# Kernel tuning notes

Measured on AMD Instinct MI355X. Metric: run time of the kernel, lower is better.

Reference implementation:

```python
import jax, jax.numpy as jnp
import numpy as np
import math

D_MODEL = 1024
N_HEADS = 16
HEAD_DIM = D_MODEL // N_HEADS
BATCH = 2
SEQ = 2048


def setup_inputs() -> dict:
    key = jax.random.key(0)
    ks = jax.random.split(key, 6)
    x = jax.random.normal(ks[0], (BATCH, SEQ, D_MODEL), dtype=jnp.float32)
    # causal additive mask, finite large negative
    causal = jnp.tril(jnp.ones((SEQ, SEQ), dtype=bool))
    attn_mask = jnp.where(causal, 0.0, -1e9).astype(jnp.float32)[None, None, :, :]
    s = 1.0 / math.sqrt(D_MODEL)
    W_qkv = jax.random.uniform(ks[1], (3 * D_MODEL, D_MODEL), jnp.float32, -s, s)
    b_qkv = jax.random.uniform(ks[2], (3 * D_MODEL,), jnp.float32, -s, s)
    W_out = jax.random.uniform(ks[3], (D_MODEL, D_MODEL), jnp.float32, -s, s)
    b_out = jax.random.uniform(ks[4], (D_MODEL,), jnp.float32, -s, s)
    return {"x": x, "attn_mask": attn_mask, "W_qkv": W_qkv, "b_qkv": b_qkv,
            "W_out": W_out, "b_out": b_out}


def reference(x, attn_mask, W_qkv, b_qkv, W_out, b_out):
    batch, seq, _ = x.shape
    # torch Linear: x @ W^T + b
    qkv = x @ W_qkv.T + b_qkv                              # [B,S,3D]
    qkv = qkv.reshape(batch, seq, 3, N_HEADS, HEAD_DIM)
    qkv = jnp.transpose(qkv, (2, 0, 3, 1, 4))              # [3,B,H,S,hd]
    q, k, v = qkv[0], qkv[1], qkv[2]
    scores = jnp.einsum('bhsd,bhtd->bhst', q, k) / math.sqrt(HEAD_DIM)
    scores = scores + attn_mask
    attn = jax.nn.softmax(scores, axis=-1)                 # dropout p=0 (eval)
    context = jnp.einsum('bhst,bhtd->bhsd', attn, v)       # [B,H,S,hd]
    context = jnp.transpose(context, (0, 2, 1, 3)).reshape(batch, seq, D_MODEL)
    return context @ W_out.T + b_out
```

## Files before the change

### kernel.cpp

```cpp
#include <hip/hip_runtime.h>
#include <hip/hip_bf16.h>

#define BATCH 2
#define SEQ 2048
#define DMODEL 1024
#define NHEADS 16
#define HDIM 64
#define MROWS (BATCH*SEQ)

typedef short bf16x8_t __attribute__((ext_vector_type(8)));
typedef float f32x4_t __attribute__((ext_vector_type(4)));

union Frag { uint4 u; bf16x8_t b; };

__device__ __forceinline__ unsigned short f2bf(float f) {
  union { __hip_bfloat16 h; unsigned short s; } u;
  u.h = __float2bfloat16(f);
  return u.s;
}

__device__ __forceinline__ void gload16(const unsigned short* g, unsigned short* l) {
  __builtin_amdgcn_global_load_lds(
      (const __attribute__((address_space(1))) unsigned int*)(const void*)g,
      (__attribute__((address_space(3))) unsigned int*)(void*)l,
      16, 0, 0);
}

__global__ void cvt_kernel(const float* __restrict__ in,
                           unsigned short* __restrict__ out, int n4) {
  for (int i = blockIdx.x * blockDim.x + threadIdx.x; i < n4;
       i += gridDim.x * blockDim.x) {
    float4 v = reinterpret_cast<const float4*>(in)[i];
    ushort4 o;
    o.x = f2bf(v.x); o.y = f2bf(v.y); o.z = f2bf(v.z); o.w = f2bf(v.w);
    reinterpret_cast<ushort4*>(out)[i] = o;
  }
}

#define QSCALE 0.18033688011112042f


__launch_bounds__(256)
__global__ void qkv_gemm_kernel(const unsigned short* __restrict__ A,
                                const unsigned short* __restrict__ Bw,
                                const float* __restrict__ bias,
                                unsigned short* __restrict__ qb,
                                unsigned short* __restrict__ kb,
                                unsigned short* __restrict__ vb) {
  __shared__ __align__(16) unsigned short As[128 * 32];
  __shared__ __align__(16) unsigned short Bs[128 * 32];
  const int tid = threadIdx.x;
  const int w = tid >> 6, lane = tid & 63;
  const int rr = lane & 15, cg = lane >> 4;
  const int wr = w >> 1, wc = w & 1;
  const int bm = blockIdx.x * 128, bn = blockIdx.y * 128;

  const int cid0 = (w * 2) * 64 + lane, cid1 = (w * 2 + 1) * 64 + lane;
  const int rowA0 = cid0 >> 2, kc0 = cid0 & 3;
  const int rowA1 = cid1 >> 2, kc1 = cid1 & 3;
  const unsigned short* gA0 = A + (size_t)(bm + rowA0) * DMODEL + kc0 * 8;
  const unsigned short* gA1 = A + (size_t)(bm + rowA1) * DMODEL + kc1 * 8;
  const unsigned short* gB0 = Bw + (size_t)(bn + rowA0) * DMODEL + kc0 * 8;
  const unsigned short* gB1 = Bw + (size_t)(bn + rowA1) * DMODEL + kc1 * 8;
  unsigned short* lA0 = As + (w * 2) * 512;
  unsigned short* lA1 = As + (w * 2 + 1) * 512;
  unsigned short* lB0 = Bs + (w * 2) * 512;
  unsigned short* lB1 = Bs + (w * 2 + 1) * 512;

  f32x4_t acc[4][4];
#pragma unroll
  for (int i = 0; i < 4; ++i)
#pragma unroll
    for (int j = 0; j < 4; ++j) acc[i][j] = (f32x4_t){0.f, 0.f, 0.f, 0.f};

  for (int k0 = 0; k0 < DMODEL; k0 += 32) {
    __syncthreads();
    gload16(gA0 + k0, lA0);
    gload16(gA1 + k0, lA1);
    gload16(gB0 + k0, lB0);
    gload16(gB1 + k0, lB1);
    __syncthreads();
    const uint4* A4 = reinterpret_cast<const uint4*>(As);
    const uint4* B4 = reinterpret_cast<const uint4*>(Bs);
    Frag af[4], bf[4];
#pragma unroll
    for (int mt = 0; mt < 4; ++mt) af[mt].u = A4[(wr * 64 + 16 * mt + rr) * 4 + cg];
#pragma unroll
    for (int nt = 0; nt < 4; ++nt) bf[nt].u = B4[(wc * 64 + 16 * nt + rr) * 4 + cg];
#pragma unroll
    for (int mt = 0; mt < 4; ++mt)
#pragma unroll
      for (int nt = 0; nt < 4; ++nt)
        acc[mt][nt] = __builtin_amdgcn_mfma_f32_16x16x32_bf16(af[mt].b, bf[nt].b, acc[mt][nt], 0, 0, 0);
  }

#pragma unroll
  for (int nt = 0; nt < 4; ++nt) {
    const int m = bn + wc * 64 + 16 * nt + rr;
    const float bv = bias[m];
    const int which = m >> 10;
    const int h = (m & 1023) >> 6;
    const int d = m & 63;
#pragma unroll
    for (int mt = 0; mt < 4; ++mt) {
#pragma unroll
      for (int r = 0; r < 4; ++r) {
        const int n = bm + wr * 64 + 16 * mt + cg * 4 + r;
        const int b = n >> 11, sq = n & (SEQ - 1);
        const int bh = b * NHEADS + h;
        float val = acc[mt][nt][r] + bv;
        if (which == 0) {
          qb[((size_t)bh * SEQ + sq) * HDIM + d] = f2bf(val * QSCALE);
        } else if (which == 1) {
          kb[((size_t)bh * SEQ + sq) * HDIM + d] = f2bf(val);
        } else {
          vb[((size_t)bh * HDIM + d) * SEQ + sq] = f2bf(val);
        }
      }
    }
  }
}

__launch_bounds__(256)
__global__ void out_gemm_kernel(const unsigned short* __restrict__ A,
                                const unsigned short* __restrict__ Bw,
                                const float* __restrict__ bias,
                                float* __restrict__ out) {
  __shared__ __align__(16) unsigned short As[128 * 32];
  __shared__ __align__(16) unsigned short Bs[128 * 32];
  const int tid = threadIdx.x;
  const int w = tid >> 6, lane = tid & 63;
  const int rr = lane & 15, cg = lane >> 4;
  const int wr = w >> 1, wc = w & 1;
  const int bm = blockIdx.x * 128, bn = blockIdx.y * 128;

  const int cid0 = (w * 2) * 64 + lane, cid1 = (w * 2 + 1) * 64 + lane;
  const int rowA0 = cid0 >> 2, kc0 = cid0 & 3;
  const int rowA1 = cid1 >> 2, kc1 = cid1 & 3;
  const unsigned short* gA0 = A + (size_t)(bm + rowA0) * DMODEL + kc0 * 8;
  const unsigned short* gA1 = A + (size_t)(bm + rowA1) * DMODEL + kc1 * 8;
  const unsigned short* gB0 = Bw + (size_t)(bn + rowA0) * DMODEL + kc0 * 8;
  const unsigned short* gB1 = Bw + (size_t)(bn + rowA1) * DMODEL + kc1 * 8;
  unsigned short* lA0 = As + (w * 2) * 512;
  unsigned short* lA1 = As + (w * 2 + 1) * 512;
  unsigned short* lB0 = Bs + (w * 2) * 512;
  unsigned short* lB1 = Bs + (w * 2 + 1) * 512;

  f32x4_t acc[4][4];
#pragma unroll
  for (int i = 0; i < 4; ++i)
#pragma unroll
    for (int j = 0; j < 4; ++j) acc[i][j] = (f32x4_t){0.f, 0.f, 0.f, 0.f};

  for (int k0 = 0; k0 < DMODEL; k0 += 32) {
    __syncthreads();
    gload16(gA0 + k0, lA0);
    gload16(gA1 + k0, lA1);
    gload16(gB0 + k0, lB0);
    gload16(gB1 + k0, lB1);
    __syncthreads();
    const uint4* A4 = reinterpret_cast<const uint4*>(As);
    const uint4* B4 = reinterpret_cast<const uint4*>(Bs);
    Frag af[4], bf[4];
#pragma unroll
    for (int mt = 0; mt < 4; ++mt) af[mt].u = A4[(wr * 64 + 16 * mt + rr) * 4 + cg];
#pragma unroll
    for (int nt = 0; nt < 4; ++nt) bf[nt].u = B4[(wc * 64 + 16 * nt + rr) * 4 + cg];
#pragma unroll
    for (int mt = 0; mt < 4; ++mt)
#pragma unroll
      for (int nt = 0; nt < 4; ++nt)
        acc[mt][nt] = __builtin_amdgcn_mfma_f32_16x16x32_bf16(af[mt].b, bf[nt].b, acc[mt][nt], 0, 0, 0);
  }

#pragma unroll
  for (int nt = 0; nt < 4; ++nt) {
    const int m = bn + wc * 64 + 16 * nt + rr;
    const float bv = bias[m];
#pragma unroll
    for (int mt = 0; mt < 4; ++mt) {
#pragma unroll
      for (int r = 0; r < 4; ++r) {
        const int n = bm + wr * 64 + 16 * mt + cg * 4 + r;
        out[(size_t)n * DMODEL + m] = acc[mt][nt][r] + bv;
      }
    }
  }
}

__launch_bounds__(256)
__global__ void attn_kernel(const unsigned short* __restrict__ qb,
                            const unsigned short* __restrict__ kb,
                            const unsigned short* __restrict__ vb,
                            unsigned short* __restrict__ ctx) {
  __shared__ __align__(16) uint4 Ks[2][512];
  __shared__ __align__(16) uint4 Vs[2][512];
  __shared__ __align__(16) uint4 Ps[4][128];

  const int tid = threadIdx.x;
  const int w = tid >> 6, lane = tid & 63;
  const int rr = lane & 15, cg = lane >> 4;
  const int rxw = rr & 7;
  const int p = blockIdx.x;
  const int bh = blockIdx.y;

  const unsigned short* Kbh = kb + (size_t)bh * SEQ * HDIM;
  const unsigned short* Vbh = vb + (size_t)bh * HDIM * SEQ;

  const int j0 = w * 2, j1 = w * 2 + 1;
  const int cid0 = j0 * 64 + lane, cid1 = j1 * 64 + lane;
  const int row0 = cid0 >> 3, ch0 = cid0 & 7;
  const int row1 = cid1 >> 3, ch1 = cid1 & 7;
  const int kOff0 = row0 * HDIM + ((ch0 ^ (row0 & 7)) << 3);
  const int kOff1 = row1 * HDIM + ((ch1 ^ (row1 & 7)) << 3);
  const int vOff0 = row0 * SEQ + ((ch0 ^ (row0 & 7)) << 3);
  const int vOff1 = row1 * SEQ + ((ch1 ^ (row1 & 7)) << 3);

  unsigned short* Pw16 = (unsigned short*)&Ps[w][0];
  const uint4* PwU4 = &Ps[w][0];

#define STAGE(bi, tb_) do {                                             \
    const unsigned short* Kt_ = Kbh + (size_t)(tb_) * HDIM;             \
    const unsigned short* Vt_ = Vbh + (tb_);                            \
    unsigned short* kl_ = (unsigned short*)&Ks[bi][0];                  \
    unsigned short* vl_ = (unsigned short*)&Vs[bi][0];                  \
    gload16(Kt_ + kOff0, kl_ + j0 * 512);                               \
    gload16(Kt_ + kOff1, kl_ + j1 * 512);                               \
    gload16(Vt_ + vOff0, vl_ + j0 * 512);                               \
    gload16(Vt_ + vOff1, vl_ + j1 * 512);                               \
  } while (0)

  const int b = bh >> 4, h = bh & 15;

  for (int ci = 0; ci < 2; ++ci) {
    const int c = (ci == 0) ? p : 31 - p;
    const int s_base = c * 64 + w * 16;
    const int nt = c + 1;

    __syncthreads();
    STAGE(0, 0);

    Frag q0, q1;
    {
      const unsigned short* qrow = qb + ((size_t)bh * SEQ + (s_base + rr)) * HDIM;
      q0.u = *reinterpret_cast<const uint4*>(qrow + cg * 8);
      q1.u = *reinterpret_cast<const uint4*>(qrow + 32 + cg * 8);
    }

    f32x4_t acc[4];
#pragma unroll
    for (int i = 0; i < 4; ++i) acc[i] = (f32x4_t){0.f, 0.f, 0.f, 0.f};
    float mreg[4] = {-1e30f, -1e30f, -1e30f, -1e30f};
    float lp[4] = {0.f, 0.f, 0.f, 0.f};

    for (int t = 0; t < nt; ++t) {
      const int tb = t * 64;
      __syncthreads();
      if (t + 1 < nt) STAGE((t + 1) & 1, (t + 1) * 64);
      if (tb > s_base + 15) continue;
      const bool last = (t == nt - 1);
      const uint4* Kt = &Ks[t & 1][0];
      const uint4* Vt = &Vs[t & 1][0];

      f32x4_t s[4];
      __builtin_amdgcn_s_setprio(1);
#pragma unroll
      for (int st = 0; st < 4; ++st) {
        s[st] = (f32x4_t){0.f, 0.f, 0.f, 0.f};
        Frag kf;
        kf.u = Kt[(st * 16 + rr) * 8 + (cg ^ rxw)];
        s[st] = __builtin_amdgcn_mfma_f32_16x16x32_bf16(q0.b, kf.b, s[st], 0, 0, 0);
        kf.u = Kt[(st * 16 + rr) * 8 + ((4 + cg) ^ rxw)];
        s[st] = __builtin_amdgcn_mfma_f32_16x16x32_bf16(q1.b, kf.b, s[st], 0, 0, 0);
      }
      __builtin_amdgcn_s_setprio(0);

      if (last) {
#pragma unroll
        for (int st = 0; st < 4; ++st) {
          const int keyl = st * 16 + rr;
#pragma unroll
          for (int r = 0; r < 4; ++r)
            if (keyl > w * 16 + cg * 4 + r) s[st][r] = -1e30f;
        }
      }

      float mx[4];
      int need = 0;
#pragma unroll
      for (int r = 0; r < 4; ++r) {
        mx[r] = fmaxf(fmaxf(s[0][r], s[1][r]), fmaxf(s[2][r], s[3][r]));
        need |= (mx[r] > mreg[r] + 11.0f);
      }
      if (__any(need)) {
#pragma unroll
        for (int r = 0; r < 4; ++r) {
          float m = mx[r];
#pragma unroll
          for (int o = 1; o < 16; o <<= 1) m = fmaxf(m, __shfl_xor(m, o));
          m = fmaxf(m, mreg[r]);
          const float alpha = exp2f(mreg[r] - m);
          mreg[r] = m;
          lp[r] *= alpha;
#pragma unroll
          for (int dt = 0; dt < 4; ++dt) acc[dt][r] *= alpha;
        }
      }
#pragma unroll
      for (int r = 0; r < 4; ++r) {
        const float p0 = exp2f(s[0][r] - mreg[r]);
        const float p1 = exp2f(s[1][r] - mreg[r]);
        const float p2 = exp2f(s[2][r] - mreg[r]);
        const float p3 = exp2f(s[3][r] - mreg[r]);
        lp[r] += (p0 + p1) + (p2 + p3);
        const int prow = cg * 4 + r;
        unsigned short* Pr = Pw16 + prow * 64;
        const int swz = (prow & 7) << 3;
        Pr[(rr)      ^ swz] = f2bf(p0);
        Pr[(rr + 16) ^ swz] = f2bf(p1);
        Pr[(rr + 32) ^ swz] = f2bf(p2);
        Pr[(rr + 48) ^ swz] = f2bf(p3);
      }

      Frag pf0, pf1;
      pf0.u = PwU4[rr * 8 + (cg ^ rxw)];
      pf1.u = PwU4[rr * 8 + ((4 + cg) ^ rxw)];
      __builtin_amdgcn_s_setprio(1);
#pragma unroll
      for (int dt = 0; dt < 4; ++dt) {
        Frag vf;
        vf.u = Vt[(dt * 16 + rr) * 8 + (cg ^ rxw)];
        acc[dt] = __builtin_amdgcn_mfma_f32_16x16x32_bf16(pf0.b, vf.b, acc[dt], 0, 0, 0);
        vf.u = Vt[(dt * 16 + rr) * 8 + ((4 + cg) ^ rxw)];
        acc[dt] = __builtin_amdgcn_mfma_f32_16x16x32_bf16(pf1.b, vf.b, acc[dt], 0, 0, 0);
      }
      __builtin_amdgcn_s_setprio(0);
    }

#pragma unroll
    for (int r = 0; r < 4; ++r) {
      float ls = lp[r];
#pragma unroll
      for (int o = 1; o < 16; o <<= 1) ls += __shfl_xor(ls, o);
      const float inv = 1.0f / ls;
      const int sq = s_base + cg * 4 + r;
      unsigned short* crow = ctx + (size_t)(b * SEQ + sq) * DMODEL + h * HDIM;
#pragma unroll
      for (int dt = 0; dt < 4; ++dt)
        crow[dt * 16 + rr] = f2bf(acc[dt][r] * inv);
    }
  }
#undef STAGE
}

extern "C" void kernel_launch(void* const* d_in, const int* in_sizes, int n_in,
                              void* d_out, int out_size, void* d_ws, size_t ws_size,
                              hipStream_t stream) {
  const float* x    = (const float*)d_in[0];
  const float* Wqkv = (const float*)d_in[2];
  const float* bqkv = (const float*)d_in[3];
  const float* Wout = (const float*)d_in[4];
  const float* bout = (const float*)d_in[5];
  float* out = (float*)d_out;

  unsigned short* ws    = (unsigned short*)d_ws;
  unsigned short* xb    = ws;
  unsigned short* wqkvb = xb + (size_t)MROWS * DMODEL;
  unsigned short* woutb = wqkvb + (size_t)3 * DMODEL * DMODEL;
  unsigned short* qbuf  = woutb + (size_t)DMODEL * DMODEL;
  unsigned short* kbuf  = qbuf + (size_t)BATCH * NHEADS * SEQ * HDIM;
  unsigned short* vbuf  = kbuf + (size_t)BATCH * NHEADS * SEQ * HDIM;
  unsigned short* ctx   = vbuf + (size_t)BATCH * NHEADS * SEQ * HDIM;

  cvt_kernel<<<1024, 256, 0, stream>>>(x, xb, MROWS * DMODEL / 4);
  cvt_kernel<<<1024, 256, 0, stream>>>(Wqkv, wqkvb, 3 * DMODEL * DMODEL / 4);
  cvt_kernel<<<256, 256, 0, stream>>>(Wout, woutb, DMODEL * DMODEL / 4);

  qkv_gemm_kernel<<<dim3(MROWS / 128, 3 * DMODEL / 128), 256, 0, stream>>>(
      xb, wqkvb, bqkv, qbuf, kbuf, vbuf);

  attn_kernel<<<dim3(SEQ / 128, BATCH * NHEADS), 256, 0, stream>>>(
      qbuf, kbuf, vbuf, ctx);

  out_gemm_kernel<<<dim3(MROWS / 128, DMODEL / 128), 256, 0, stream>>>(
      ctx, woutb, bout, out);
}
```

Measured before the change: 131.4 us.

## Compute transposed S in attention, pass P via permlane swaps, one chunk per block

```diff
diff --git a/kernel.cpp b/kernel.cpp
--- a/kernel.cpp
+++ b/kernel.cpp
@@ -188,21 +188,20 @@
   }
 }
 
-__launch_bounds__(256)
+__launch_bounds__(256, 4)
 __global__ void attn_kernel(const unsigned short* __restrict__ qb,
                             const unsigned short* __restrict__ kb,
                             const unsigned short* __restrict__ vb,
                             unsigned short* __restrict__ ctx) {
   __shared__ __align__(16) uint4 Ks[2][512];
   __shared__ __align__(16) uint4 Vs[2][512];
-  __shared__ __align__(16) uint4 Ps[4][128];
 
   const int tid = threadIdx.x;
   const int w = tid >> 6, lane = tid & 63;
   const int rr = lane & 15, cg = lane >> 4;
   const int rxw = rr & 7;
-  const int p = blockIdx.x;
-  const int bh = blockIdx.y;
+  const int bh = blockIdx.x;
+  const int c = 31 - blockIdx.y;
 
   const unsigned short* Kbh = kb + (size_t)bh * SEQ * HDIM;
   const unsigned short* Vbh = vb + (size_t)bh * HDIM * SEQ;
@@ -215,9 +214,6 @@
   const int kOff1 = row1 * HDIM + ((ch1 ^ (row1 & 7)) << 3);
   const int vOff0 = row0 * SEQ + ((ch0 ^ (row0 & 7)) << 3);
   const int vOff1 = row1 * SEQ + ((ch1 ^ (row1 & 7)) << 3);
-
-  unsigned short* Pw16 = (unsigned short*)&Ps[w][0];
-  const uint4* PwU4 = &Ps[w][0];
 
 #define STAGE(bi, tb_) do {                                             \
     const unsigned short* Kt_ = Kbh + (size_t)(tb_) * HDIM;             \
@@ -231,124 +227,127 @@
   } while (0)
 
   const int b = bh >> 4, h = bh & 15;
-
-  for (int ci = 0; ci < 2; ++ci) {
-    const int c = (ci == 0) ? p : 31 - p;
-    const int s_base = c * 64 + w * 16;
-    const int nt = c + 1;
-
-    __syncthreads();
-    STAGE(0, 0);
-
-    Frag q0, q1;
-    {
-      const unsigned short* qrow = qb + ((size_t)bh * SEQ + (s_base + rr)) * HDIM;
-      q0.u = *reinterpret_cast<const uint4*>(qrow + cg * 8);
-      q1.u = *reinterpret_cast<const uint4*>(qrow + 32 + cg * 8);
-    }
-
-    f32x4_t acc[4];
-#pragma unroll
-    for (int i = 0; i < 4; ++i) acc[i] = (f32x4_t){0.f, 0.f, 0.f, 0.f};
-    float mreg[4] = {-1e30f, -1e30f, -1e30f, -1e30f};
-    float lp[4] = {0.f, 0.f, 0.f, 0.f};
-
-    for (int t = 0; t < nt; ++t) {
-      const int tb = t * 64;
-      __syncthreads();
-      if (t + 1 < nt) STAGE((t + 1) & 1, (t + 1) * 64);
-      if (tb > s_base + 15) continue;
-      const bool last = (t == nt - 1);
-      const uint4* Kt = &Ks[t & 1][0];
-      const uint4* Vt = &Vs[t & 1][0];
-
-      f32x4_t s[4];
-      __builtin_amdgcn_s_setprio(1);
-#pragma unroll
-      for (int st = 0; st < 4; ++st) {
-        s[st] = (f32x4_t){0.f, 0.f, 0.f, 0.f};
-        Frag kf;
-        kf.u = Kt[(st * 16 + rr) * 8 + (cg ^ rxw)];
-        s[st] = __builtin_amdgcn_mfma_f32_16x16x32_bf16(q0.b, kf.b, s[st], 0, 0, 0);
-        kf.u = Kt[(st * 16 + rr) * 8 + ((4 + cg) ^ rxw)];
-        s[st] = __builtin_amdgcn_mfma_f32_16x16x32_bf16(q1.b, kf.b, s[st], 0, 0, 0);
+  const int s_base = c * 64 + w * 16;
+  const int nt = c + 1;
+
+  STAGE(0, 0);
+
+  Frag q0, q1;
+  {
+    const unsigned short* qrow = qb + ((size_t)bh * SEQ + (s_base + rr)) * HDIM;
+    q0.u = *reinterpret_cast<const uint4*>(qrow + cg * 8);
+    q1.u = *reinterpret_cast<const uint4*>(qrow + 32 + cg * 8);
+  }
+
+  f32x4_t acc[4];
+#pragma unroll
+  for (int i = 0; i < 4; ++i) acc[i] = (f32x4_t){0.f, 0.f, 0.f, 0.f};
+  float mreg = -1e30f;
+  float lp = 0.f;
+
+  for (int t = 0; t < nt; ++t) {
+    __syncthreads();
+    if (t + 1 < nt) STAGE((t + 1) & 1, (t + 1) * 64);
+    const uint4* Kt = &Ks[t & 1][0];
+    const uint4* Vt = &Vs[t & 1][0];
+
+    f32x4_t s[4];
+    __builtin_amdgcn_s_setprio(1);
+#pragma unroll
+    for (int st = 0; st < 4; ++st) {
+      s[st] = (f32x4_t){0.f, 0.f, 0.f, 0.f};
+      Frag kf;
+      kf.u = Kt[(st * 16 + rr) * 8 + (cg ^ rxw)];
+      s[st] = __builtin_amdgcn_mfma_f32_16x16x32_bf16(kf.b, q0.b, s[st], 0, 0, 0);
+      kf.u = Kt[(st * 16 + rr) * 8 + ((4 + cg) ^ rxw)];
+      s[st] = __builtin_amdgcn_mfma_f32_16x16x32_bf16(kf.b, q1.b, s[st], 0, 0, 0);
+    }
+    __builtin_amdgcn_s_setprio(0);
+
+    if (t == nt - 1) {
+#pragma unroll
+      for (int st = 0; st < 4; ++st)
+#pragma unroll
+        for (int r = 0; r < 4; ++r)
+          if (st * 16 + cg * 4 + r > w * 16 + rr) s[st][r] = -1e30f;
+    }
+
+    float mx = s[0][0];
+#pragma unroll
+    for (int st = 0; st < 4; ++st)
+#pragma unroll
+      for (int r = 0; r < 4; ++r) mx = fmaxf(mx, s[st][r]);
+    if (__any(mx > mreg + 11.0f)) {
+      float m = fmaxf(mx, __shfl_xor(mx, 16));
+      m = fmaxf(m, __shfl_xor(m, 32));
+      m = fmaxf(m, mreg);
+      const float alpha = exp2f(mreg - m);
+      mreg = m;
+      lp *= alpha;
+      float av[4];
+#pragma unroll
+      for (int r = 0; r < 4; ++r) av[r] = __shfl(alpha, cg * 4 + r);
+#pragma unroll
+      for (int dt = 0; dt < 4; ++dt)
+#pragma unroll
+        for (int r = 0; r < 4; ++r) acc[dt][r] *= av[r];
+    }
+
+    float pv[4][4];
+#pragma unroll
+    for (int st = 0; st < 4; ++st)
+#pragma unroll
+      for (int r = 0; r < 4; ++r) {
+        pv[st][r] = exp2f(s[st][r] - mreg);
+        lp += pv[st][r];
       }
-      __builtin_amdgcn_s_setprio(0);
-
-      if (last) {
-#pragma unroll
-        for (int st = 0; st < 4; ++st) {
-          const int keyl = st * 16 + rr;
-#pragma unroll
-          for (int r = 0; r < 4; ++r)
-            if (keyl > w * 16 + cg * 4 + r) s[st][r] = -1e30f;
-        }
+
+    unsigned int uu[4][2];
+#pragma unroll
+    for (int st = 0; st < 4; ++st)
+#pragma unroll
+      for (int i = 0; i < 2; ++i)
+        asm("v_cvt_pk_bf16_f32 %0, %1, %2"
+            : "=v"(uu[st][i]) : "v"(pv[st][2 * i]), "v"(pv[st][2 * i + 1]));
+
+    Frag pA0, pA1;
+#pragma unroll
+    for (int s2 = 0; s2 < 2; ++s2) {
+#pragma unroll
+      for (int i = 0; i < 2; ++i) {
+        unsigned int x = uu[2 * s2][i], y = uu[2 * s2 + 1][i];
+        asm("v_permlane32_swap_b32 %0, %1" : "+v"(x), "+v"(y));
+        asm("v_permlane16_swap_b32 %0, %1" : "+v"(x), "+v"(y));
+        if (s2 == 0) { pA0.u[i] = x; pA0.u[2 + i] = y; }
+        else         { pA1.u[i] = x; pA1.u[2 + i] = y; }
       }
-
-      float mx[4];
-      int need = 0;
-#pragma unroll
-      for (int r = 0; r < 4; ++r) {
-        mx[r] = fmaxf(fmaxf(s[0][r], s[1][r]), fmaxf(s[2][r], s[3][r]));
-        need |= (mx[r] > mreg[r] + 11.0f);
-      }
-      if (__any(need)) {
-#pragma unroll
-        for (int r = 0; r < 4; ++r) {
-          float m = mx[r];
-#pragma unroll
-          for (int o = 1; o < 16; o <<= 1) m = fmaxf(m, __shfl_xor(m, o));
-          m = fmaxf(m, mreg[r]);
-          const float alpha = exp2f(mreg[r] - m);
-          mreg[r] = m;
-          lp[r] *= alpha;
-#pragma unroll
-          for (int dt = 0; dt < 4; ++dt) acc[dt][r] *= alpha;
-        }
-      }
-#pragma unroll
-      for (int r = 0; r < 4; ++r) {
-        const float p0 = exp2f(s[0][r] - mreg[r]);
-        const float p1 = exp2f(s[1][r] - mreg[r]);
-        const float p2 = exp2f(s[2][r] - mreg[r]);
-        const float p3 = exp2f(s[3][r] - mreg[r]);
-        lp[r] += (p0 + p1) + (p2 + p3);
-        const int prow = cg * 4 + r;
-        unsigned short* Pr = Pw16 + prow * 64;
-        const int swz = (prow & 7) << 3;
-        Pr[(rr)      ^ swz] = f2bf(p0);
-        Pr[(rr + 16) ^ swz] = f2bf(p1);
-        Pr[(rr + 32) ^ swz] = f2bf(p2);
-        Pr[(rr + 48) ^ swz] = f2bf(p3);
-      }
-
-      Frag pf0, pf1;
-      pf0.u = PwU4[rr * 8 + (cg ^ rxw)];
-      pf1.u = PwU4[rr * 8 + ((4 + cg) ^ rxw)];
-      __builtin_amdgcn_s_setprio(1);
-#pragma unroll
-      for (int dt = 0; dt < 4; ++dt) {
-        Frag vf;
-        vf.u = Vt[(dt * 16 + rr) * 8 + (cg ^ rxw)];
-        acc[dt] = __builtin_amdgcn_mfma_f32_16x16x32_bf16(pf0.b, vf.b, acc[dt], 0, 0, 0);
-        vf.u = Vt[(dt * 16 + rr) * 8 + ((4 + cg) ^ rxw)];
-        acc[dt] = __builtin_amdgcn_mfma_f32_16x16x32_bf16(pf1.b, vf.b, acc[dt], 0, 0, 0);
-      }
-      __builtin_amdgcn_s_setprio(0);
-    }
-
-#pragma unroll
-    for (int r = 0; r < 4; ++r) {
-      float ls = lp[r];
-#pragma unroll
-      for (int o = 1; o < 16; o <<= 1) ls += __shfl_xor(ls, o);
-      const float inv = 1.0f / ls;
-      const int sq = s_base + cg * 4 + r;
-      unsigned short* crow = ctx + (size_t)(b * SEQ + sq) * DMODEL + h * HDIM;
-#pragma unroll
-      for (int dt = 0; dt < 4; ++dt)
-        crow[dt * 16 + rr] = f2bf(acc[dt][r] * inv);
-    }
+    }
+
+    __builtin_amdgcn_s_setprio(1);
+#pragma unroll
+    for (int dt = 0; dt < 4; ++dt) {
+      Frag vf;
+      vf.u = Vt[(dt * 16 + rr) * 8 + (cg ^ rxw)];
+      acc[dt] = __builtin_amdgcn_mfma_f32_16x16x32_bf16(pA0.b, vf.b, acc[dt], 0, 0, 0);
+      vf.u = Vt[(dt * 16 + rr) * 8 + ((4 + cg) ^ rxw)];
+      acc[dt] = __builtin_amdgcn_mfma_f32_16x16x32_bf16(pA1.b, vf.b, acc[dt], 0, 0, 0);
+    }
+    __builtin_amdgcn_s_setprio(0);
+  }
+
+  float ls = lp + __shfl_xor(lp, 16);
+  ls += __shfl_xor(ls, 32);
+  const float inv = 1.0f / ls;
+  float iv[4];
+#pragma unroll
+  for (int r = 0; r < 4; ++r) iv[r] = __shfl(inv, cg * 4 + r);
+#pragma unroll
+  for (int r = 0; r < 4; ++r) {
+    const int sq = s_base + cg * 4 + r;
+    unsigned short* crow = ctx + (size_t)(b * SEQ + sq) * DMODEL + h * HDIM;
+#pragma unroll
+    for (int dt = 0; dt < 4; ++dt)
+      crow[dt * 16 + rr] = f2bf(acc[dt][r] * iv[r]);
   }
 #undef STAGE
 }
@@ -379,7 +378,7 @@
   qkv_gemm_kernel<<<dim3(MROWS / 128, 3 * DMODEL / 128), 256, 0, stream>>>(
       xb, wqkvb, bqkv, qbuf, kbuf, vbuf);
 
-  attn_kernel<<<dim3(SEQ / 128, BATCH * NHEADS), 256, 0, stream>>>(
+  attn_kernel<<<dim3(BATCH * NHEADS, SEQ / 64), 256, 0, stream>>>(
       qbuf, kbuf, vbuf, ctx);
 
   out_gemm_kernel<<<dim3(MROWS / 128, DMODEL / 128), 256, 0, stream>>>(
```

Measured after the change: 114.8 us. -12.6%, faster.
